# Kernel optimization log

Hardware: AMD Instinct MI355X
Metric: run time of the kernel (lower is better)

## Reference

```python
import jax, jax.numpy as jnp
import numpy as np

B, N, M, D = 8, 4096, 4096, 2


def setup_inputs() -> dict:
    key = jax.random.key(0)
    k1, k2 = jax.random.split(key)
    x = jax.random.normal(k1, (B, N, D), dtype=jnp.float32)
    target = jax.random.normal(k2, (B, M, D), dtype=jnp.float32)
    return {"x": x, "target": target}


def reference(x, target):
    # Pairwise squared Euclidean distances [B, N, M] via the expansion
    # ||a-b||^2 = ||a||^2 + ||b||^2 - 2 a.b  (matmul-friendly form).
    x2 = jnp.sum(x * x, axis=-1)            # [B, N]
    t2 = jnp.sum(target * target, axis=-1)  # [B, M]
    cross = jnp.einsum("bnd,bmd->bnm", x, target)  # [B, N, M]
    d2 = x2[:, :, None] + t2[:, None, :] - 2.0 * cross
    d2 = jnp.maximum(d2, 0.0)  # numerical floor before sqrt
    # tree1.query(array2[i]): for each target point, distance to nearest x point.
    d_t_to_x = jnp.sqrt(jnp.min(d2, axis=1))  # [B, M]
    # tree2.query(array1[i]): for each x point, distance to nearest target point.
    d_x_to_t = jnp.sqrt(jnp.min(d2, axis=2))  # [B, N]
    # sum over batch of (mean1 + mean2)/B == mean of per-batch means (equal sizes).
    return jnp.mean(d_t_to_x) + jnp.mean(d_x_to_t)
```

## Files before the change

kernel.cpp:

```cpp
#include <hip/hip_runtime.h>
#include <math.h>

#define NPTS   4096
#define BQ     256
#define RQ     8
#define SLOTS  (BQ / RQ)
#define NS     (1024 / SLOTS)
#define CHUNK  (NPTS / NS)

__global__ __launch_bounds__(1024) void chamfer_main(
    const float* __restrict__ x, const float* __restrict__ tgt,
    float* __restrict__ partials)
{
    __shared__ float4 sm[NPTS / 2];
    __shared__ float  mins[NS * BQ];

    const int bx  = blockIdx.x;
    const int dir = bx >> 7;
    const int b   = (bx >> 4) & 7;
    const int qt  = bx & 15;
    const int tid = threadIdx.x;

    const float* qarr = dir ? tgt : x;
    const float* sarr = dir ? x   : tgt;

    const float4* sp4 = (const float4*)(sarr + b * (NPTS * 2));
    for (int k = tid; k < NPTS / 2; k += 1024) sm[k] = sp4[k];

    const int slot = tid & (SLOTS - 1);
    const int s    = tid >> 5;
    const float2* qp = (const float2*)(qarr + b * (NPTS * 2));
    float nx[RQ], ny[RQ], pp[RQ], m[RQ];
    #pragma unroll
    for (int r = 0; r < RQ; ++r) {
        const float2 p = qp[qt * BQ + slot + r * SLOTS];
        nx[r] = -2.f * p.x;
        ny[r] = -2.f * p.y;
        pp[r] = fmaf(p.x, p.x, p.y * p.y);
        m[r]  = INFINITY;
    }

    __syncthreads();

    const float4* tp = sm + s * (CHUNK / 2);
    #pragma unroll 4
    for (int j = 0; j < CHUNK / 2; ++j) {
        const float4 t = tp[j];
        const float z0 = fmaf(t.x, t.x, t.y * t.y);
        const float z1 = fmaf(t.z, t.z, t.w * t.w);
        #pragma unroll
        for (int r = 0; r < RQ; ++r) {
            m[r] = fminf(m[r], fmaf(nx[r], t.x, fmaf(ny[r], t.y, z0)));
            m[r] = fminf(m[r], fmaf(nx[r], t.z, fmaf(ny[r], t.w, z1)));
        }
    }

    #pragma unroll
    for (int r = 0; r < RQ; ++r)
        mins[s * BQ + slot + r * SLOTS] = m[r] + pp[r];
    __syncthreads();

    float dval = 0.f;
    if (tid < BQ) {
        float mm = mins[tid];
        #pragma unroll
        for (int ss = 1; ss < NS; ++ss) mm = fminf(mm, mins[ss * BQ + tid]);
        dval = sqrtf(fmaxf(mm, 0.f));
    }
    __syncthreads();
    float* red = (float*)sm;
    if (tid < BQ) red[tid] = dval;
    __syncthreads();
    if (tid < 64) {
        float v = red[tid] + red[tid + 64] + red[tid + 128] + red[tid + 192];
        v += __shfl_down(v, 32);
        v += __shfl_down(v, 16);
        v += __shfl_down(v, 8);
        v += __shfl_down(v, 4);
        v += __shfl_down(v, 2);
        v += __shfl_down(v, 1);
        if (tid == 0) partials[blockIdx.x] = v;
    }
}

__global__ __launch_bounds__(256) void chamfer_final(
    const float* __restrict__ partials, float* __restrict__ out)
{
    __shared__ float red[256];
    const int tid = threadIdx.x;
    red[tid] = partials[tid];
    __syncthreads();
    if (tid < 64) {
        float v = red[tid] + red[tid + 64] + red[tid + 128] + red[tid + 192];
        v += __shfl_down(v, 32);
        v += __shfl_down(v, 16);
        v += __shfl_down(v, 8);
        v += __shfl_down(v, 4);
        v += __shfl_down(v, 2);
        v += __shfl_down(v, 1);
        if (tid == 0) out[0] = v * (1.0f / 32768.0f);
    }
}

extern "C" void kernel_launch(void* const* d_in, const int* in_sizes, int n_in,
                              void* d_out, int out_size, void* d_ws, size_t ws_size,
                              hipStream_t stream) {
    const float* x   = (const float*)d_in[0];
    const float* tgt = (const float*)d_in[1];
    float* partials  = (float*)d_ws;
    float* out       = (float*)d_out;

    chamfer_main<<<dim3(256), dim3(1024), 0, stream>>>(x, tgt, partials);
    chamfer_final<<<dim3(1), dim3(256), 0, stream>>>(partials, out);
}
```

Before: 24.61 us.

## Repartition chamfer into smaller query tiles with shuffle-based min reduction

Splits the work into 1024 blocks of 512 threads, each handling 64 queries with 16 per thread and 128 source slices of 32 points, instead of 256 blocks of 1024 threads. The shared source array is padded to avoid bank conflicts, and the cross-slice min runs through wave shuffles before a small shared reduction. The aim is more blocks per CU and better load balance across the GPU's 256 CUs, plus cheaper reduction. The cost is that each block reloads the full 32KB source set into shared memory, so there are 4x more redundant global and LDS loads, and register pressure rises with RQ=16.

```diff
diff --git a/kernel.cpp b/kernel.cpp
--- a/kernel.cpp
+++ b/kernel.cpp
@@ -1,85 +1,95 @@
 #include <hip/hip_runtime.h>
 #include <math.h>
 
-#define NPTS   4096
-#define BQ     256
-#define RQ     8
-#define SLOTS  (BQ / RQ)
-#define NS     (1024 / SLOTS)
-#define CHUNK  (NPTS / NS)
+#define NPTS  4096
+#define BQ    64
+#define RQ    16
+#define SLOTS 4
+#define NS    128
+#define CHUNK 32
+#define CF4   16
+#define PCF4  17
 
-__global__ __launch_bounds__(1024) void chamfer_main(
+__global__ __launch_bounds__(512, 6) void chamfer_main(
     const float* __restrict__ x, const float* __restrict__ tgt,
     float* __restrict__ partials)
 {
-    __shared__ float4 sm[NPTS / 2];
-    __shared__ float  mins[NS * BQ];
+    __shared__ float4 sm[NS * PCF4];
+    __shared__ float  red[8 * BQ];
 
     const int bx  = blockIdx.x;
-    const int dir = bx >> 7;
-    const int b   = (bx >> 4) & 7;
-    const int qt  = bx & 15;
-    const int tid = threadIdx.x;
+    const int dir = bx >> 9;
+    const int b   = (bx >> 6) & 7;
+    const int qt  = bx & 63;
+    const int t   = threadIdx.x;
+    const int lane = t & 63, w = t >> 6;
 
     const float* qarr = dir ? tgt : x;
     const float* sarr = dir ? x   : tgt;
 
     const float4* sp4 = (const float4*)(sarr + b * (NPTS * 2));
-    for (int k = tid; k < NPTS / 2; k += 1024) sm[k] = sp4[k];
+    #pragma unroll
+    for (int k = 0; k < 4; ++k) {
+        const int i = t + k * 512;
+        sm[i + (i >> 4)] = sp4[i];
+    }
 
-    const int slot = tid & (SLOTS - 1);
-    const int s    = tid >> 5;
+    const int slot = t & (SLOTS - 1);
+    const int s    = t >> 2;
     const float2* qp = (const float2*)(qarr + b * (NPTS * 2));
-    float nx[RQ], ny[RQ], pp[RQ], m[RQ];
+    float nx[RQ], ny[RQ], m[RQ];
     #pragma unroll
     for (int r = 0; r < RQ; ++r) {
-        const float2 p = qp[qt * BQ + slot + r * SLOTS];
+        const float2 p = qp[qt * BQ + slot + SLOTS * r];
         nx[r] = -2.f * p.x;
         ny[r] = -2.f * p.y;
-        pp[r] = fmaf(p.x, p.x, p.y * p.y);
         m[r]  = INFINITY;
     }
-
     __syncthreads();
 
-    const float4* tp = sm + s * (CHUNK / 2);
+    const float4* tp = sm + s * PCF4;
     #pragma unroll 4
-    for (int j = 0; j < CHUNK / 2; ++j) {
-        const float4 t = tp[j];
-        const float z0 = fmaf(t.x, t.x, t.y * t.y);
-        const float z1 = fmaf(t.z, t.z, t.w * t.w);
+    for (int j = 0; j < CF4; ++j) {
+        const float4 t4 = tp[j];
+        const float z0 = fmaf(t4.x, t4.x, t4.y * t4.y);
+        const float z1 = fmaf(t4.z, t4.z, t4.w * t4.w);
         #pragma unroll
         for (int r = 0; r < RQ; ++r) {
-            m[r] = fminf(m[r], fmaf(nx[r], t.x, fmaf(ny[r], t.y, z0)));
-            m[r] = fminf(m[r], fmaf(nx[r], t.z, fmaf(ny[r], t.w, z1)));
+            const float d0 = fmaf(nx[r], t4.x, fmaf(ny[r], t4.y, z0));
+            const float d1 = fmaf(nx[r], t4.z, fmaf(ny[r], t4.w, z1));
+            m[r] = fminf(fminf(m[r], d0), d1);
         }
     }
 
     #pragma unroll
     for (int r = 0; r < RQ; ++r)
-        mins[s * BQ + slot + r * SLOTS] = m[r] + pp[r];
+        m[r] += 0.25f * fmaf(nx[r], nx[r], ny[r] * ny[r]);
+
+    #pragma unroll
+    for (int r = 0; r < RQ; ++r) {
+        m[r] = fminf(m[r], __shfl_xor(m[r], 4));
+        m[r] = fminf(m[r], __shfl_xor(m[r], 8));
+        m[r] = fminf(m[r], __shfl_xor(m[r], 16));
+        m[r] = fminf(m[r], __shfl_xor(m[r], 32));
+    }
+    if (lane < SLOTS) {
+        #pragma unroll
+        for (int r = 0; r < RQ; ++r) red[w * BQ + lane + SLOTS * r] = m[r];
+    }
     __syncthreads();
 
-    float dval = 0.f;
-    if (tid < BQ) {
-        float mm = mins[tid];
+    if (t < BQ) {
+        float mm = red[t];
         #pragma unroll
-        for (int ss = 1; ss < NS; ++ss) mm = fminf(mm, mins[ss * BQ + tid]);
-        dval = sqrtf(fmaxf(mm, 0.f));
-    }
-    __syncthreads();
-    float* red = (float*)sm;
-    if (tid < BQ) red[tid] = dval;
-    __syncthreads();
-    if (tid < 64) {
-        float v = red[tid] + red[tid + 64] + red[tid + 128] + red[tid + 192];
+        for (int ww = 1; ww < 8; ++ww) mm = fminf(mm, red[ww * BQ + t]);
+        float v = sqrtf(fmaxf(mm, 0.f));
         v += __shfl_down(v, 32);
         v += __shfl_down(v, 16);
         v += __shfl_down(v, 8);
         v += __shfl_down(v, 4);
         v += __shfl_down(v, 2);
         v += __shfl_down(v, 1);
-        if (tid == 0) partials[blockIdx.x] = v;
+        if (t == 0) partials[bx] = v;
     }
 }
 
@@ -88,17 +98,19 @@
 {
     __shared__ float red[256];
     const int tid = threadIdx.x;
-    red[tid] = partials[tid];
+    float v = partials[tid] + partials[tid + 256] +
+              partials[tid + 512] + partials[tid + 768];
+    red[tid] = v;
     __syncthreads();
     if (tid < 64) {
-        float v = red[tid] + red[tid + 64] + red[tid + 128] + red[tid + 192];
-        v += __shfl_down(v, 32);
-        v += __shfl_down(v, 16);
-        v += __shfl_down(v, 8);
-        v += __shfl_down(v, 4);
-        v += __shfl_down(v, 2);
-        v += __shfl_down(v, 1);
-        if (tid == 0) out[0] = v * (1.0f / 32768.0f);
+        float s = red[tid] + red[tid + 64] + red[tid + 128] + red[tid + 192];
+        s += __shfl_down(s, 32);
+        s += __shfl_down(s, 16);
+        s += __shfl_down(s, 8);
+        s += __shfl_down(s, 4);
+        s += __shfl_down(s, 2);
+        s += __shfl_down(s, 1);
+        if (tid == 0) out[0] = s * (1.0f / 32768.0f);
     }
 }
 
@@ -110,6 +122,6 @@
     float* partials  = (float*)d_ws;
     float* out       = (float*)d_out;
 
-    chamfer_main<<<dim3(256), dim3(1024), 0, stream>>>(x, tgt, partials);
-    chamfer_final<<<dim3(1), dim3(256), 0, stream>>>(partials, out);
+    chamfer_main<<<dim3(1024), dim3(512), 0, stream>>>(x, tgt, partials);
+    chamfer_final<<<dim3(1),   dim3(256), 0, stream>>>(partials, out);
 }
```

Result: slower. 26.24 us (+6.6%).
